# Optimization experiments

Hardware: AMD Instinct MI355X
Metric: run time of the kernel (lower is better)

## Reference

```python
import jax, jax.numpy as jnp
import numpy as np

NX = 768
N_HEAD = 12
N_CTX = 2048
MASKED_BIAS = -10000.0


def setup_inputs() -> dict:
    key = jax.random.key(0)
    ks = jax.random.split(key, 6)
    bs, seq = 2, N_CTX
    hidden_states = jax.random.normal(ks[0], (bs, seq, NX), dtype=jnp.float32)
    attention_mask = jnp.zeros((bs, 1, 1, seq), dtype=jnp.float32)
    # Conv1D params: out = x @ W + b, W: (in, out)
    w_attn = jax.random.normal(ks[1], (NX, 3 * NX), dtype=jnp.float32) * 0.02
    b_attn = jnp.zeros((3 * NX,), dtype=jnp.float32)
    w_proj = jax.random.normal(ks[2], (NX, NX), dtype=jnp.float32) * 0.02
    b_proj = jnp.zeros((NX,), dtype=jnp.float32)
    return {
        "hidden_states": hidden_states,
        "attention_mask": attention_mask,
        "w_attn": w_attn,
        "b_attn": b_attn,
        "w_proj": w_proj,
        "b_proj": b_proj,
    }


def reference(hidden_states, attention_mask, w_attn, b_attn, w_proj, b_proj):
    bs, seq, _ = hidden_states.shape
    hd = NX // N_HEAD  # 64
    qkv = hidden_states @ w_attn + b_attn  # [bs, seq, 3*nx]
    query, key, value = jnp.split(qkv, 3, axis=2)
    # Faithful to source: direct reshape (NOT standard split-heads transpose)
    q = query.reshape(bs, N_HEAD, seq, hd)
    k = key.reshape(bs, N_HEAD, seq, hd)
    v = value.reshape(bs, N_HEAD, seq, hd)
    w = jnp.einsum("bhqd,bhkd->bhqk", q, k) / jnp.sqrt(jnp.float32(hd))
    # causal mask: tril, sliced as bias[:, :, ns-nd:ns, :ns] with nd=ns=seq
    mask = jnp.tril(jnp.ones((seq, seq), dtype=jnp.float32))[None, None]
    w = w * mask + MASKED_BIAS * (1.0 - mask)
    w = w + attention_mask
    w = jax.nn.softmax(w, axis=-1)  # dropout = identity (eval mode)
    a = jnp.einsum("bhqk,bhkd->bhqd", w, v)
    a = a.transpose(0, 2, 1, 3).reshape(bs, seq, NX)
    a = a @ w_proj + b_proj  # resid dropout = identity
    return a
```

## Files before the change

kernel.cpp:

```cpp
#include <hip/hip_runtime.h>
#include <hip/hip_bf16.h>

typedef unsigned short u16;
typedef short bf16x8 __attribute__((ext_vector_type(8)));
typedef float f32x4 __attribute__((ext_vector_type(4)));

#define NXC 768
#define NHEAD 12
#define SEQ 2048
#define BSZ 2
#define HD 64
#define NCHUNK 40
#define LOG2E 1.4426950408889634f

__device__ inline u16 f2bf(float f) {
    unsigned int u = __float_as_uint(f);
    unsigned int r = u + 0x7fffu + ((u >> 16) & 1u);
    return (u16)(r >> 16);
}
__device__ inline unsigned pk2(float lo, float hi) {
    return (unsigned)f2bf(lo) | ((unsigned)f2bf(hi) << 16);
}
__device__ inline float ex2(float x) { return __builtin_amdgcn_exp2f(x); }

__device__ inline void gld16(const u16* g, u16* l) {
    __builtin_amdgcn_global_load_lds(
        (const __attribute__((address_space(1))) unsigned int*)(g),
        (__attribute__((address_space(3))) unsigned int*)(l),
        16, 0, 0);
}

__global__ __launch_bounds__(256) void prep_kernel(
    const float* __restrict__ hs, u16* __restrict__ HSbf,
    const float* __restrict__ w_attn, u16* __restrict__ WaT,
    const float* __restrict__ w_proj, u16* __restrict__ WpT) {
    __shared__ float tile[32][33];
    int blk = blockIdx.x;
    int t = threadIdx.x;
    if (blk < 3072) {
        int i = blk * 256 + t;
        float4 v = ((const float4*)hs)[i];
        ushort4 o;
        o.x = f2bf(v.x); o.y = f2bf(v.y); o.z = f2bf(v.z); o.w = f2bf(v.w);
        ((ushort4*)HSbf)[i] = o;
        return;
    }
    const float* in; u16* out; int C, cb, rb;
    if (blk < 4800) {
        int idx = blk - 3072;
        in = w_attn; out = WaT; C = 3 * NXC;
        cb = (idx % 72) * 32; rb = (idx / 72) * 32;
    } else {
        int idx = blk - 4800;
        in = w_proj; out = WpT; C = NXC;
        cb = (idx % 24) * 32; rb = (idx / 24) * 32;
    }
    int tx = t & 31, ty = t >> 5;
    #pragma unroll
    for (int i = 0; i < 32; i += 8)
        tile[ty + i][tx] = in[(size_t)(rb + ty + i) * C + cb + tx];
    __syncthreads();
    #pragma unroll
    for (int i = 0; i < 32; i += 8)
        out[(size_t)(cb + ty + i) * NXC + rb + tx] = f2bf(tile[tx][ty + i]);
}

__global__ __launch_bounds__(256) void vt_kernel(const u16* __restrict__ Vb,
                                                 u16* __restrict__ Vtg) {
    __shared__ u16 tile[64][68];
    int y = blockIdx.y;
    size_t base = (size_t)y * (SEQ * HD);
    int ss0 = blockIdx.x * 64;
    int t = threadIdx.x;
    #pragma unroll
    for (int c = t; c < 512; c += 256) {
        int r = c >> 3, col = (c & 7) * 8;
        *(uint4*)&tile[r][col] = *(const uint4*)&Vb[base + (size_t)(ss0 + r) * HD + col];
    }
    __syncthreads();
    #pragma unroll
    for (int c = t; c < 512; c += 256) {
        int dd = c >> 3, s8 = (c & 7) * 8;
        ushort4 a, bq;
        a.x = tile[s8 + 0][dd]; a.y = tile[s8 + 1][dd];
        a.z = tile[s8 + 2][dd]; a.w = tile[s8 + 3][dd];
        bq.x = tile[s8 + 4][dd]; bq.y = tile[s8 + 5][dd];
        bq.z = tile[s8 + 6][dd]; bq.w = tile[s8 + 7][dd];
        u16* dst = &Vtg[base + (size_t)dd * SEQ + ss0 + s8];
        *(ushort4*)dst = a;
        *(ushort4*)(dst + 4) = bq;
    }
}

template <int EPI>
__global__ __launch_bounds__(256) void gemm_bt_kernel(
    const u16* __restrict__ A, const u16* __restrict__ BT,
    const float* __restrict__ bias,
    u16* __restrict__ outQ, u16* __restrict__ outK, u16* __restrict__ outV,
    float* __restrict__ outF,
    int M, int N, int K) {
    __shared__ u16 As[3 * 128 * 32];
    __shared__ u16 Bs[3 * 128 * 32];
    int numN = N >> 7, numM = M >> 7;
    int nPer = numN >> 1, mPer = numM >> 2;
    int wgid = blockIdx.x;
    int xcd = wgid & 7, local = wgid >> 3;
    int nloc = local % nPer, mloc = local / nPer;
    int tileN = (((xcd & 1) * nPer) + nloc) << 7;
    int tileM = ((((xcd >> 1) & 3) * mPer) + mloc) << 7;
    int t = threadIdx.x;
    int lane = t & 63, wave = t >> 6;
    int wr = (wave >> 1) * 64, wc = (wave & 1) * 64;
    int quad = lane >> 4, l16 = lane & 15;
    f32x4 acc[4][4] = {};

    int r0 = t >> 2, c0 = (t & 3) * 8;
    const u16* Ag0 = A + (size_t)(tileM + r0) * K + c0;
    const u16* Ag1 = Ag0 + (size_t)64 * K;
    const u16* Bg0 = BT + (size_t)(tileN + r0) * K + c0;
    const u16* Bg1 = Bg0 + (size_t)64 * K;
    u16* AsW0 = As + wave * 512;
    u16* AsW1 = As + 2048 + wave * 512;
    u16* BsW0 = Bs + wave * 512;
    u16* BsW1 = Bs + 2048 + wave * 512;

    gld16(Ag0, AsW0);
    gld16(Ag1, AsW1);
    gld16(Bg0, BsW0);
    gld16(Bg1, BsW1);
    gld16(Ag0 + 32, AsW0 + 4096);
    gld16(Ag1 + 32, AsW1 + 4096);
    gld16(Bg0 + 32, BsW0 + 4096);
    gld16(Bg1 + 32, BsW1 + 4096);

    int NT = K >> 5;
    for (int tt = 0; tt < NT; ++tt) {
        int cur = tt % 3;
        if (tt + 2 < NT) {
            int kn = (tt + 2) * 32;
            int nb = ((tt + 2) % 3) * 4096;
            gld16(Ag0 + kn, AsW0 + nb);
            gld16(Ag1 + kn, AsW1 + nb);
            gld16(Bg0 + kn, BsW0 + nb);
            gld16(Bg1 + kn, BsW1 + nb);
            asm volatile("s_waitcnt vmcnt(8)" ::: "memory");
        } else if (tt + 1 < NT) {
            asm volatile("s_waitcnt vmcnt(4)" ::: "memory");
        } else {
            asm volatile("s_waitcnt vmcnt(0)" ::: "memory");
        }
        __builtin_amdgcn_s_barrier();
        __builtin_amdgcn_sched_barrier(0);

        const u16* Ac = As + cur * 4096;
        const u16* Bc = Bs + cur * 4096;
        bf16x8 af[4], bfr[4];
        #pragma unroll
        for (int i = 0; i < 4; ++i)
            af[i] = *(const bf16x8*)&Ac[(wr + i * 16 + l16) * 32 + quad * 8];
        #pragma unroll
        for (int j = 0; j < 4; ++j)
            bfr[j] = *(const bf16x8*)&Bc[(wc + j * 16 + l16) * 32 + quad * 8];
        #pragma unroll
        for (int i = 0; i < 4; ++i)
            #pragma unroll
            for (int j = 0; j < 4; ++j)
                acc[i][j] = __builtin_amdgcn_mfma_f32_16x16x32_bf16(af[i], bfr[j], acc[i][j], 0, 0, 0);

        __builtin_amdgcn_sched_barrier(0);
        __builtin_amdgcn_s_barrier();
    }

    #pragma unroll
    for (int i = 0; i < 4; ++i) {
        #pragma unroll
        for (int j = 0; j < 4; ++j) {
            int n = tileN + wc + j * 16 + l16;
            float bv = bias[n];
            #pragma unroll
            for (int r = 0; r < 4; ++r) {
                int m = tileM + wr + i * 16 + quad * 4 + r;
                float v = acc[i][j][r] + bv;
                if (EPI == 0) {
                    if (n < 768) {
                        outQ[(size_t)m * 768 + n] = f2bf(v);
                    } else if (n < 1536) {
                        outK[(size_t)m * 768 + (n - 768)] = f2bf(v * (0.125f * LOG2E));
                    } else {
                        outV[(size_t)m * 768 + (n - 1536)] = f2bf(v);
                    }
                } else {
                    outF[(size_t)m * N + n] = v;
                }
            }
        }
    }
}

__global__ __launch_bounds__(512) void attn_mfma_kernel(
    const u16* __restrict__ Q, const u16* __restrict__ Kg,
    const u16* __restrict__ Vtg, const float* __restrict__ amask,
    u16* __restrict__ Opart, float* __restrict__ Lpart) {
    __shared__ u16 Ks[64][72];
    __shared__ u16 Vt[64][72];
    __shared__ u16 Ps[8][16][72];
    __shared__ float Ams[64];

    int wgid = blockIdx.x;
    int xcd = wgid & 7, local = wgid >> 3;
    int bh = xcd * 3 + local / NCHUNK;
    int px = local % NCHUNK;
    int b = bh / NHEAD, h = bh % NHEAD;
    int p = NCHUNK - 1 - px;
    int bx = 15, c = 0, a = 0;
    #pragma unroll
    for (int i = 0; i < 16; ++i) {
        int n = (i >> 2) + 1;
        if (p < a + n) { bx = i; c = p - a; break; }
        a += n;
    }
    int kbase = c * 512;
    int nt = 2 * (bx + 1) - 8 * c;
    if (nt > 8) nt = 8;

    int t = threadIdx.x;
    int w = t >> 6, lane = t & 63;
    int quad = lane >> 4, l16 = lane & 15;
    size_t headbase = (size_t)b * (SEQ * NXC) + (size_t)h * (SEQ * HD);
    size_t headbaseT = (size_t)(b * NHEAD + h) * (SEQ * HD);

    int r0 = bx * 128;
    int qw0 = r0 + w * 16;
    int qrow = qw0 + l16;
    bf16x8 qf[2];
    #pragma unroll
    for (int s = 0; s < 2; ++s)
        qf[s] = *(const bf16x8*)&Q[headbase + (size_t)(qw0 + l16) * HD + s * 32 + quad * 8];

    float l_part = 0.f;
    f32x4 o[4] = {};

    int pr_row = t >> 3, pr_col = (t & 7) * 8;
    uint4 kr, vr; float amr;
    {
        int k0 = kbase;
        kr = *(const uint4*)&Kg[headbase + (size_t)(k0 + pr_row) * HD + pr_col];
        vr = *(const uint4*)&Vtg[headbaseT + (size_t)pr_row * SEQ + k0 + pr_col];
        if (t < 64) amr = amask[(size_t)b * SEQ + k0 + t];
    }

    for (int kt = 0; kt < nt; ++kt) {
        int k0 = kbase + kt * 64;
        __syncthreads();
        *(uint4*)&Ks[pr_row][pr_col] = kr;
        *(uint4*)&Vt[pr_row][pr_col] = vr;
        if (t < 64) Ams[t] = amr * LOG2E;
        __syncthreads();
        if (kt + 1 < nt) {
            int kn = k0 + 64;
            kr = *(const uint4*)&Kg[headbase + (size_t)(kn + pr_row) * HD + pr_col];
            vr = *(const uint4*)&Vtg[headbaseT + (size_t)pr_row * SEQ + kn + pr_col];
            if (t < 64) amr = amask[(size_t)b * SEQ + kn + t];
        }

        if (k0 > qw0 + 15) continue;

        bf16x8 kf[2][4];
        #pragma unroll
        for (int s = 0; s < 2; ++s)
            #pragma unroll
            for (int j = 0; j < 4; ++j)
                kf[s][j] = *(const bf16x8*)&Ks[j * 16 + l16][s * 32 + quad * 8];
        f32x4 amv4[4];
        #pragma unroll
        for (int j = 0; j < 4; ++j)
            amv4[j] = *(const f32x4*)&Ams[j * 16 + quad * 4];

        f32x4 sacc[4] = {};
        __builtin_amdgcn_s_setprio(1);
        #pragma unroll
        for (int s = 0; s < 2; ++s)
            #pragma unroll
            for (int j = 0; j < 4; ++j)
                sacc[j] = __builtin_amdgcn_mfma_f32_16x16x32_bf16(kf[s][j], qf[s], sacc[j], 0, 0, 0);
        __builtin_amdgcn_s_setprio(0);

        bool diag = (k0 + 63 > qw0);
        #pragma unroll
        for (int j = 0; j < 4; ++j) {
            float pv[4];
            #pragma unroll
            for (int r = 0; r < 4; ++r) {
                float pp = ex2(sacc[j][r] + amv4[j][r]);
                if (diag && (k0 + j * 16 + quad * 4 + r > qrow)) pp = 0.f;
                pv[r] = pp;
            }
            l_part += (pv[0] + pv[1]) + (pv[2] + pv[3]);
            __hip_bfloat162 h01 = __float22bfloat162_rn(make_float2(pv[0], pv[1]));
            __hip_bfloat162 h23 = __float22bfloat162_rn(make_float2(pv[2], pv[3]));
            uint2 u;
            __builtin_memcpy(&u.x, &h01, 4);
            __builtin_memcpy(&u.y, &h23, 4);
            *(uint2*)&Ps[w][l16][j * 16 + quad * 4] = u;
        }

        __builtin_amdgcn_s_setprio(1);
        #pragma unroll
        for (int s = 0; s < 2; ++s) {
            bf16x8 pf = *(const bf16x8*)&Ps[w][l16][s * 32 + quad * 8];
            #pragma unroll
            for (int dc = 0; dc < 4; ++dc) {
                bf16x8 vf = *(const bf16x8*)&Vt[dc * 16 + l16][s * 32 + quad * 8];
                o[dc] = __builtin_amdgcn_mfma_f32_16x16x32_bf16(pf, vf, o[dc], 0, 0, 0);
            }
        }
        __builtin_amdgcn_s_setprio(0);
    }

    float l = l_part + __shfl_xor(l_part, 16);
    l += __shfl_xor(l, 32);
    u16* Ob = Opart + ((size_t)bh * NCHUNK + p) * (128 * 64);
    float* Lb = Lpart + ((size_t)bh * NCHUNK + p) * 128;
    #pragma unroll
    for (int dc = 0; dc < 4; ++dc)
        #pragma unroll
        for (int r = 0; r < 4; ++r) {
            int rl = w * 16 + quad * 4 + r;
            Ob[rl * 64 + dc * 16 + l16] = f2bf(o[dc][r]);
        }
    if (quad == 0) Lb[w * 16 + l16] = l;
}

__global__ __launch_bounds__(256) void attn_combine_kernel(
    const u16* __restrict__ Opart, const float* __restrict__ Lpart,
    u16* __restrict__ Aout) {
    __shared__ float winv[32];
    int bh = blockIdx.y;
    int b = bh / NHEAD, h = bh % NHEAD;
    int row0 = blockIdx.x * 32;
    int bx = row0 >> 7;
    int aa = bx >> 2, bb = bx & 3;
    int nch = aa + 1;
    int p0 = (aa + 1) * (2 * aa + bb);
    int rbase = row0 & 127;
    int t = threadIdx.x;

    if (t < 32) {
        float L = 0.f;
        for (int c = 0; c < nch; ++c)
            L += Lpart[((size_t)bh * NCHUNK + p0 + c) * 128 + rbase + t];
        winv[t] = 1.0f / L;
    }
    __syncthreads();

    int row = t >> 3;
    int d0 = (t & 7) * 8;
    int rl = rbase + row;
    float acc[8] = {};
    for (int c = 0; c < nch; ++c) {
        uint4 u = *(const uint4*)&Opart[(((size_t)bh * NCHUNK + p0 + c) * 128 + rl) * 64 + d0];
        acc[0] += __uint_as_float(u.x << 16);
        acc[1] += __uint_as_float(u.x & 0xffff0000u);
        acc[2] += __uint_as_float(u.y << 16);
        acc[3] += __uint_as_float(u.y & 0xffff0000u);
        acc[4] += __uint_as_float(u.z << 16);
        acc[5] += __uint_as_float(u.z & 0xffff0000u);
        acc[6] += __uint_as_float(u.w << 16);
        acc[7] += __uint_as_float(u.w & 0xffff0000u);
    }
    float s = winv[row];
    uint4 o;
    o.x = pk2(acc[0] * s, acc[1] * s);
    o.y = pk2(acc[2] * s, acc[3] * s);
    o.z = pk2(acc[4] * s, acc[5] * s);
    o.w = pk2(acc[6] * s, acc[7] * s);
    *(uint4*)&Aout[((size_t)b * SEQ + row0 + row) * NXC + h * HD + d0] = o;
}

extern "C" void kernel_launch(void* const* d_in, const int* in_sizes, int n_in,
                              void* d_out, int out_size, void* d_ws, size_t ws_size,
                              hipStream_t stream) {
    const float* hs     = (const float*)d_in[0];
    const float* amask  = (const float*)d_in[1];
    const float* w_attn = (const float*)d_in[2];
    const float* b_attn = (const float*)d_in[3];
    const float* w_proj = (const float*)d_in[4];
    const float* b_proj = (const float*)d_in[5];
    float* out = (float*)d_out;

    const int M = BSZ * SEQ;
    char* ws = (char*)d_ws;
    auto alloc = [&](size_t bytes) {
        char* p = ws;
        ws += (bytes + 255) & ~(size_t)255;
        return p;
    };
    u16* HSbf   = (u16*)alloc((size_t)M * NXC * 2);
    u16* WaT    = (u16*)alloc((size_t)3 * NXC * NXC * 2);
    u16* WpT    = (u16*)alloc((size_t)NXC * NXC * 2);
    u16* Qb     = (u16*)alloc((size_t)M * NXC * 2);
    u16* Kb     = (u16*)alloc((size_t)M * NXC * 2);
    u16* Vb     = (u16*)alloc((size_t)M * NXC * 2);
    u16* Vtg    = (u16*)alloc((size_t)M * NXC * 2);
    u16* Ab     = (u16*)alloc((size_t)M * NXC * 2);
    u16* Opart  = (u16*)alloc((size_t)BSZ * NHEAD * NCHUNK * 128 * 64 * 2);
    float* Lpart = (float*)alloc((size_t)BSZ * NHEAD * NCHUNK * 128 * 4);

    prep_kernel<<<dim3(5376), dim3(256), 0, stream>>>(hs, HSbf, w_attn, WaT, w_proj, WpT);
    gemm_bt_kernel<0><<<dim3((3 * NXC / 128) * (M / 128)), dim3(256), 0, stream>>>(
        HSbf, WaT, b_attn, Qb, Kb, Vb, nullptr, M, 3 * NXC, NXC);
    vt_kernel<<<dim3(SEQ / 64, BSZ * NHEAD), dim3(256), 0, stream>>>(Vb, Vtg);
    attn_mfma_kernel<<<dim3(NCHUNK * BSZ * NHEAD), dim3(512), 0, stream>>>(
        Qb, Kb, Vtg, amask, Opart, Lpart);
    attn_combine_kernel<<<dim3(SEQ / 32, BSZ * NHEAD), dim3(256), 0, stream>>>(
        Opart, Lpart, Ab);
    gemm_bt_kernel<1><<<dim3((NXC / 128) * (M / 128)), dim3(256), 0, stream>>>(
        Ab, WpT, b_proj, nullptr, nullptr, nullptr, out, M, NXC, NXC);
}
```

Baseline: 172.0 us.

## Halve attention block to 4 waves with 32 query rows each

The attention kernel now runs 256 threads per block, and each wave handles two 16-row query groups, so every K fragment read from LDS feeds two MFMAs. The causal skip is tracked per group. The attention mask is now read straight from global memory, with the LOG2E scaling folded into an fma, and the LDS staging for the mask is removed. This cuts LDS traffic per MFMA and the number of waves per block, at the cost of more registers per wave and fewer waves available to hide latency.

```diff
diff --git a/kernel.cpp b/kernel.cpp
--- a/kernel.cpp
+++ b/kernel.cpp
@@ -197,14 +197,13 @@
     }
 }
 
-__global__ __launch_bounds__(512) void attn_mfma_kernel(
+__global__ __launch_bounds__(256) void attn_mfma_kernel(
     const u16* __restrict__ Q, const u16* __restrict__ Kg,
     const u16* __restrict__ Vtg, const float* __restrict__ amask,
     u16* __restrict__ Opart, float* __restrict__ Lpart) {
     __shared__ u16 Ks[64][72];
     __shared__ u16 Vt[64][72];
-    __shared__ u16 Ps[8][16][72];
-    __shared__ float Ams[64];
+    __shared__ u16 Ps[4][2][16][72];
 
     int wgid = blockIdx.x;
     int xcd = wgid & 7, local = wgid >> 3;
@@ -229,106 +228,125 @@
     size_t headbase = (size_t)b * (SEQ * NXC) + (size_t)h * (SEQ * HD);
     size_t headbaseT = (size_t)(b * NHEAD + h) * (SEQ * HD);
 
-    int r0 = bx * 128;
-    int qw0 = r0 + w * 16;
-    int qrow = qw0 + l16;
-    bf16x8 qf[2];
-    #pragma unroll
-    for (int s = 0; s < 2; ++s)
-        qf[s] = *(const bf16x8*)&Q[headbase + (size_t)(qw0 + l16) * HD + s * 32 + quad * 8];
-
-    float l_part = 0.f;
-    f32x4 o[4] = {};
-
-    int pr_row = t >> 3, pr_col = (t & 7) * 8;
-    uint4 kr, vr; float amr;
+    int qw0 = bx * 128 + w * 32;
+    bf16x8 qf[2][2];
+    #pragma unroll
+    for (int g = 0; g < 2; ++g)
+        #pragma unroll
+        for (int s = 0; s < 2; ++s)
+            qf[g][s] = *(const bf16x8*)&Q[headbase +
+                (size_t)(qw0 + g * 16 + l16) * HD + s * 32 + quad * 8];
+
+    float l_part[2] = {0.f, 0.f};
+    f32x4 o[2][4] = {};
+
+    int r0a = t >> 3, c0a = (t & 7) * 8;
+    int r0b = r0a + 32;
+    uint4 kra, krb, vra, vrb;
     {
         int k0 = kbase;
-        kr = *(const uint4*)&Kg[headbase + (size_t)(k0 + pr_row) * HD + pr_col];
-        vr = *(const uint4*)&Vtg[headbaseT + (size_t)pr_row * SEQ + k0 + pr_col];
-        if (t < 64) amr = amask[(size_t)b * SEQ + k0 + t];
+        kra = *(const uint4*)&Kg[headbase + (size_t)(k0 + r0a) * HD + c0a];
+        krb = *(const uint4*)&Kg[headbase + (size_t)(k0 + r0b) * HD + c0a];
+        vra = *(const uint4*)&Vtg[headbaseT + (size_t)r0a * SEQ + k0 + c0a];
+        vrb = *(const uint4*)&Vtg[headbaseT + (size_t)r0b * SEQ + k0 + c0a];
     }
 
     for (int kt = 0; kt < nt; ++kt) {
         int k0 = kbase + kt * 64;
         __syncthreads();
-        *(uint4*)&Ks[pr_row][pr_col] = kr;
-        *(uint4*)&Vt[pr_row][pr_col] = vr;
-        if (t < 64) Ams[t] = amr * LOG2E;
+        *(uint4*)&Ks[r0a][c0a] = kra;
+        *(uint4*)&Ks[r0b][c0a] = krb;
+        *(uint4*)&Vt[r0a][c0a] = vra;
+        *(uint4*)&Vt[r0b][c0a] = vrb;
         __syncthreads();
         if (kt + 1 < nt) {
             int kn = k0 + 64;
-            kr = *(const uint4*)&Kg[headbase + (size_t)(kn + pr_row) * HD + pr_col];
-            vr = *(const uint4*)&Vtg[headbaseT + (size_t)pr_row * SEQ + kn + pr_col];
-            if (t < 64) amr = amask[(size_t)b * SEQ + kn + t];
-        }
-
-        if (k0 > qw0 + 15) continue;
-
-        bf16x8 kf[2][4];
-        #pragma unroll
-        for (int s = 0; s < 2; ++s)
+            kra = *(const uint4*)&Kg[headbase + (size_t)(kn + r0a) * HD + c0a];
+            krb = *(const uint4*)&Kg[headbase + (size_t)(kn + r0b) * HD + c0a];
+            vra = *(const uint4*)&Vtg[headbaseT + (size_t)r0a * SEQ + kn + c0a];
+            vrb = *(const uint4*)&Vtg[headbaseT + (size_t)r0b * SEQ + kn + c0a];
+        }
+
+        if (k0 > qw0 + 31) continue;
+        bool g0act = (k0 <= qw0 + 15);
+
+        f32x4 amv4[4];
+        #pragma unroll
+        for (int j = 0; j < 4; ++j)
+            amv4[j] = *(const f32x4*)&amask[(size_t)b * SEQ + k0 + j * 16 + quad * 4];
+
+        f32x4 sacc[2][4] = {};
+        __builtin_amdgcn_s_setprio(1);
+        #pragma unroll
+        for (int s = 0; s < 2; ++s) {
+            bf16x8 kf[4];
             #pragma unroll
             for (int j = 0; j < 4; ++j)
-                kf[s][j] = *(const bf16x8*)&Ks[j * 16 + l16][s * 32 + quad * 8];
-        f32x4 amv4[4];
-        #pragma unroll
-        for (int j = 0; j < 4; ++j)
-            amv4[j] = *(const f32x4*)&Ams[j * 16 + quad * 4];
-
-        f32x4 sacc[4] = {};
+                kf[j] = *(const bf16x8*)&Ks[j * 16 + l16][s * 32 + quad * 8];
+            #pragma unroll
+            for (int j = 0; j < 4; ++j) {
+                sacc[0][j] = __builtin_amdgcn_mfma_f32_16x16x32_bf16(kf[j], qf[0][s], sacc[0][j], 0, 0, 0);
+                sacc[1][j] = __builtin_amdgcn_mfma_f32_16x16x32_bf16(kf[j], qf[1][s], sacc[1][j], 0, 0, 0);
+            }
+        }
+        __builtin_amdgcn_s_setprio(0);
+
+        #pragma unroll
+        for (int g = 0; g < 2; ++g) {
+            if (g == 0 && !g0act) continue;
+            int qrow = qw0 + g * 16 + l16;
+            bool diag = (k0 + 63 > qw0 + g * 16);
+            #pragma unroll
+            for (int j = 0; j < 4; ++j) {
+                float pv[4];
+                #pragma unroll
+                for (int r = 0; r < 4; ++r) {
+                    float pp = ex2(fmaf(amv4[j][r], LOG2E, sacc[g][j][r]));
+                    if (diag && (k0 + j * 16 + quad * 4 + r > qrow)) pp = 0.f;
+                    pv[r] = pp;
+                }
+                l_part[g] += (pv[0] + pv[1]) + (pv[2] + pv[3]);
+                __hip_bfloat162 h01 = __float22bfloat162_rn(make_float2(pv[0], pv[1]));
+                __hip_bfloat162 h23 = __float22bfloat162_rn(make_float2(pv[2], pv[3]));
+                uint2 u;
+                __builtin_memcpy(&u.x, &h01, 4);
+                __builtin_memcpy(&u.y, &h23, 4);
+                *(uint2*)&Ps[w][g][l16][j * 16 + quad * 4] = u;
+            }
+        }
+
         __builtin_amdgcn_s_setprio(1);
         #pragma unroll
-        for (int s = 0; s < 2; ++s)
-            #pragma unroll
-            for (int j = 0; j < 4; ++j)
-                sacc[j] = __builtin_amdgcn_mfma_f32_16x16x32_bf16(kf[s][j], qf[s], sacc[j], 0, 0, 0);
-        __builtin_amdgcn_s_setprio(0);
-
-        bool diag = (k0 + 63 > qw0);
-        #pragma unroll
-        for (int j = 0; j < 4; ++j) {
-            float pv[4];
-            #pragma unroll
-            for (int r = 0; r < 4; ++r) {
-                float pp = ex2(sacc[j][r] + amv4[j][r]);
-                if (diag && (k0 + j * 16 + quad * 4 + r > qrow)) pp = 0.f;
-                pv[r] = pp;
-            }
-            l_part += (pv[0] + pv[1]) + (pv[2] + pv[3]);
-            __hip_bfloat162 h01 = __float22bfloat162_rn(make_float2(pv[0], pv[1]));
-            __hip_bfloat162 h23 = __float22bfloat162_rn(make_float2(pv[2], pv[3]));
-            uint2 u;
-            __builtin_memcpy(&u.x, &h01, 4);
-            __builtin_memcpy(&u.y, &h23, 4);
-            *(uint2*)&Ps[w][l16][j * 16 + quad * 4] = u;
-        }
-
-        __builtin_amdgcn_s_setprio(1);
-        #pragma unroll
         for (int s = 0; s < 2; ++s) {
-            bf16x8 pf = *(const bf16x8*)&Ps[w][l16][s * 32 + quad * 8];
+            bf16x8 pf0 = {}, pf1;
+            if (g0act) pf0 = *(const bf16x8*)&Ps[w][0][l16][s * 32 + quad * 8];
+            pf1 = *(const bf16x8*)&Ps[w][1][l16][s * 32 + quad * 8];
             #pragma unroll
             for (int dc = 0; dc < 4; ++dc) {
                 bf16x8 vf = *(const bf16x8*)&Vt[dc * 16 + l16][s * 32 + quad * 8];
-                o[dc] = __builtin_amdgcn_mfma_f32_16x16x32_bf16(pf, vf, o[dc], 0, 0, 0);
+                if (g0act)
+                    o[0][dc] = __builtin_amdgcn_mfma_f32_16x16x32_bf16(pf0, vf, o[0][dc], 0, 0, 0);
+                o[1][dc] = __builtin_amdgcn_mfma_f32_16x16x32_bf16(pf1, vf, o[1][dc], 0, 0, 0);
             }
         }
         __builtin_amdgcn_s_setprio(0);
     }
 
-    float l = l_part + __shfl_xor(l_part, 16);
-    l += __shfl_xor(l, 32);
     u16* Ob = Opart + ((size_t)bh * NCHUNK + p) * (128 * 64);
     float* Lb = Lpart + ((size_t)bh * NCHUNK + p) * 128;
     #pragma unroll
-    for (int dc = 0; dc < 4; ++dc)
-        #pragma unroll
-        for (int r = 0; r < 4; ++r) {
-            int rl = w * 16 + quad * 4 + r;
-            Ob[rl * 64 + dc * 16 + l16] = f2bf(o[dc][r]);
-        }
-    if (quad == 0) Lb[w * 16 + l16] = l;
+    for (int g = 0; g < 2; ++g) {
+        float l = l_part[g] + __shfl_xor(l_part[g], 16);
+        l += __shfl_xor(l, 32);
+        if (quad == 0) Lb[w * 32 + g * 16 + l16] = l;
+        #pragma unroll
+        for (int dc = 0; dc < 4; ++dc)
+            #pragma unroll
+            for (int r = 0; r < 4; ++r) {
+                int rl = w * 32 + g * 16 + quad * 4 + r;
+                Ob[rl * 64 + dc * 16 + l16] = f2bf(o[g][dc][r]);
+            }
+    }
 }
 
 __global__ __launch_bounds__(256) void attn_combine_kernel(
@@ -410,7 +428,7 @@
     gemm_bt_kernel<0><<<dim3((3 * NXC / 128) * (M / 128)), dim3(256), 0, stream>>>(
         HSbf, WaT, b_attn, Qb, Kb, Vb, nullptr, M, 3 * NXC, NXC);
     vt_kernel<<<dim3(SEQ / 64, BSZ * NHEAD), dim3(256), 0, stream>>>(Vb, Vtg);
-    attn_mfma_kernel<<<dim3(NCHUNK * BSZ * NHEAD), dim3(512), 0, stream>>>(
+    attn_mfma_kernel<<<dim3(NCHUNK * BSZ * NHEAD), dim3(256), 0, stream>>>(
         Qb, Kb, Vtg, amask, Opart, Lpart);
     attn_combine_kernel<<<dim3(SEQ / 32, BSZ * NHEAD), dim3(256), 0, stream>>>(
         Opart, Lpart, Ab);
```

After: 174.5 us. About the same (+1.5%).
